# Optimization experiments

Hardware: AMD Instinct MI355X
Metric: run time of the kernel (lower is better)

## Reference

```python
import jax, jax.numpy as jnp
import numpy as np

B, T, D, H = 4096, 100, 64, 128
N_RK4 = 4  # fixed RK4 substeps per observation gap (deterministic stand-in for adaptive odeint)


def setup_inputs() -> dict:
    key = jax.random.key(0)
    ks = jax.random.split(key, 12)
    x_seq = jax.random.normal(ks[0], (B, T, D), dtype=jnp.float32)
    # strictly increasing shared timestamps (source only uses t_seq[0, :])
    t0 = jnp.cumsum(jax.random.uniform(ks[1], (T,), dtype=jnp.float32) * 0.1 + 0.01)
    t_seq = jnp.broadcast_to(t0, (B, T))
    s_h = 1.0 / np.sqrt(H)
    s_d = 1.0 / np.sqrt(D)
    # ODE func: f(h) = tanh(h W1^T + b1) W2^T + b2
    W1 = jax.random.normal(ks[2], (H, H), jnp.float32) * s_h
    b1 = jnp.zeros((H,), jnp.float32)
    W2 = jax.random.normal(ks[3], (H, H), jnp.float32) * s_h * 0.1
    b2 = jnp.zeros((H,), jnp.float32)
    # GRUCell params (PyTorch layout: [3H, in])
    W_ih = jax.random.normal(ks[4], (3 * H, D), jnp.float32) * s_d
    W_hh = jax.random.normal(ks[5], (3 * H, H), jnp.float32) * s_h
    b_ih = jax.random.normal(ks[6], (3 * H,), jnp.float32) * s_h
    b_hh = jax.random.normal(ks[7], (3 * H,), jnp.float32) * s_h
    W_mu = jax.random.normal(ks[8], (H, H), jnp.float32) * s_h
    b_mu = jnp.zeros((H,), jnp.float32)
    W_lv = jax.random.normal(ks[9], (H, H), jnp.float32) * s_h
    b_lv = jnp.zeros((H,), jnp.float32)
    return dict(x_seq=x_seq, t_seq=t_seq, W1=W1, b1=b1, W2=W2, b2=b2,
                W_ih=W_ih, W_hh=W_hh, b_ih=b_ih, b_hh=b_hh,
                W_mu=W_mu, b_mu=b_mu, W_lv=W_lv, b_lv=b_lv)


def _odernn(x_seq, t_seq, W1, b1, W2, b2, W_ih, W_hh, b_ih, b_hh, W_mu, b_mu, W_lv, b_lv):
    Hdim = W1.shape[0]

    def f(h):  # ode_func, autonomous
        return jnp.tanh(h @ W1.T + b1) @ W2.T + b2

    def rk4_jump(h, dt):  # integrate dh/dt = f(h) over dt with N_RK4 substeps
        sub = dt / N_RK4  # scalar
        for _ in range(N_RK4):
            k1 = f(h)
            k2 = f(h + 0.5 * sub * k1)
            k3 = f(h + 0.5 * sub * k2)
            k4 = f(h + sub * k3)
            h = h + (sub / 6.0) * (k1 + 2.0 * k2 + 2.0 * k3 + k4)
        return h

    def gru(x, h):
        gi = x @ W_ih.T + b_ih  # [B, 3H]
        gh = h @ W_hh.T + b_hh
        i_r, i_z, i_n = jnp.split(gi, 3, axis=-1)
        h_r, h_z, h_n = jnp.split(gh, 3, axis=-1)
        r = jax.nn.sigmoid(i_r + h_r)
        z = jax.nn.sigmoid(i_z + h_z)
        n = jnp.tanh(i_n + r * h_n)
        return (1.0 - z) * n + z * h

    t0 = t_seq[0]  # [T] shared times, as in source (t_seq[0, i])
    dt = jnp.concatenate([jnp.zeros((1,), t0.dtype), t0[1:] - t0[:-1]])  # dt[0]=0 -> no jump at i=0
    h0 = jnp.zeros((x_seq.shape[0], Hdim), x_seq.dtype)

    def step(h, inp):
        x_i, dt_i = inp
        h = rk4_jump(h, dt_i)
        h = gru(x_i, h)
        return h, None

    h, _ = jax.lax.scan(step, h0, (jnp.swapaxes(x_seq, 0, 1), dt))
    mu = h @ W_mu.T + b_mu
    logvar = h @ W_lv.T + b_lv
    return mu, logvar


def reference(x_seq, t_seq, W1, b1, W2, b2, W_ih, W_hh, b_ih, b_hh, W_mu, b_mu, W_lv, b_lv):
    return _odernn(x_seq, t_seq, W1, b1, W2, b2, W_ih, W_hh, b_ih, b_hh, W_mu, b_mu, W_lv, b_lv)
```

## Files before the change

### kernel.cpp

```cpp
#include <hip/hip_runtime.h>

#define Bn 4096
#define Tn 100
#define Dn 64
#define Hn 128

typedef _Float16 half8v __attribute__((ext_vector_type(8)));
typedef _Float16 half4v __attribute__((ext_vector_type(4)));
typedef float    float4v __attribute__((ext_vector_type(4)));
typedef float    float2v __attribute__((ext_vector_type(2)));

__device__ __forceinline__ float fast_tanh(float x) {
    float e = __expf(x + x);
    return 1.0f - 2.0f * __builtin_amdgcn_rcpf(e + 1.0f);
}
__device__ __forceinline__ float fast_sig(float x) {
    return __builtin_amdgcn_rcpf(1.0f + __expf(-x));
}
__device__ __forceinline__ float4v tanh4(float4v u) {
    float4v a;
#pragma unroll
    for (int r = 0; r < 4; r++) a[r] = fast_tanh(u[r]);
    return a;
}
__device__ __forceinline__ half4v pack4(float4v v) {
    half4v p;
#pragma unroll
    for (int r = 0; r < 4; r++) p[r] = (_Float16)v[r];
    return p;
}

__device__ __forceinline__ half8v load_wfrag(const float* __restrict__ W, int ld, int n, int k) {
    const float* p = W + (size_t)n * ld + k;
    float4v a = *(const float4v*)p;
    float4v b = *(const float4v*)(p + 4);
    half8v r;
    r[0] = (_Float16)a[0]; r[1] = (_Float16)a[1]; r[2] = (_Float16)a[2]; r[3] = (_Float16)a[3];
    r[4] = (_Float16)b[0]; r[5] = (_Float16)b[1]; r[6] = (_Float16)b[2]; r[7] = (_Float16)b[3];
    return r;
}

__global__ __launch_bounds__(512) void odernn_kernel(
    const float* __restrict__ x_seq, const float* __restrict__ t_seq,
    const float* __restrict__ W1,   const float* __restrict__ b1,
    const float* __restrict__ W2,   const float* __restrict__ b2,
    const float* __restrict__ W_ih, const float* __restrict__ W_hh,
    const float* __restrict__ b_ih, const float* __restrict__ b_hh,
    const float* __restrict__ W_mu, const float* __restrict__ b_mu,
    const float* __restrict__ W_lv, const float* __restrict__ b_lv,
    float* __restrict__ out)
{
    __shared__ _Float16 vbuf[16 * 136];
    __shared__ _Float16 abuf[2][16 * 136];
    __shared__ _Float16 xbuf[16 * 72];
    __shared__ float    ts_l[Tn];
    __shared__ float    c1s[Hn];

    const int tid  = threadIdx.x;
    const int lane = tid & 63;
    const int w    = tid >> 6;
    const int q    = lane >> 4;
    const int m    = lane & 15;
    const int blk  = blockIdx.x;

    if (tid < Tn) ts_l[tid] = t_seq[tid];
    for (int i = tid; i < 16 * 136; i += 512) vbuf[i] = (_Float16)0.f;
    if (tid < Hn) {
        float acc = 0.f;
        const float* r1 = W1 + (size_t)tid * Hn;
#pragma unroll 4
        for (int j = 0; j < Hn; j++) acc += b2[j] * r1[j];
        c1s[tid] = acc;
    }

    const int n0 = 16 * w + m;
    half8v w1f[4], w2f[4], whhf[3][4], wihf[3][2];
#pragma unroll
    for (int kt = 0; kt < 4; kt++) {
        w1f[kt] = load_wfrag(W1, Hn, n0, 32 * kt + q * 8);
        w2f[kt] = load_wfrag(W2, Hn, n0, 32 * kt + q * 8);
    }
#pragma unroll
    for (int g = 0; g < 3; g++) {
        int n = 128 * g + n0;
#pragma unroll
        for (int kt = 0; kt < 4; kt++) whhf[g][kt] = load_wfrag(W_hh, Hn, n, 32 * kt + q * 8);
#pragma unroll
        for (int kt = 0; kt < 2; kt++) wihf[g][kt] = load_wfrag(W_ih, Dn, n, 32 * kt + q * 8);
    }
    float4v b1q = *(const float4v*)(b1 + 16 * w + q * 4);
    float4v b2q = *(const float4v*)(b2 + 16 * w + q * 4);
    float4v bihq[3], bhhq[3];
#pragma unroll
    for (int g = 0; g < 3; g++) {
        bihq[g] = *(const float4v*)(b_ih + 128 * g + 16 * w + q * 4);
        bhhq[g] = *(const float4v*)(b_hh + 128 * g + 16 * w + q * 4);
    }

    float4v accM[4][2];
#pragma unroll
    for (int kt = 0; kt < 4; kt++) {
        float4v zz = {0.f, 0.f, 0.f, 0.f};
        accM[kt][0] = zz; accM[kt][1] = zz;
    }
    {
        const float* w1row = W1 + (size_t)n0 * Hn;
        for (int j = 0; j < Hn; j++) {
            float w1v = w1row[j];
            const float* w2r = W2 + (size_t)j * Hn + q * 8;
#pragma unroll
            for (int kt = 0; kt < 4; kt++) {
                float4v aa = *(const float4v*)(w2r + 32 * kt);
                float4v bb = *(const float4v*)(w2r + 32 * kt + 4);
#pragma unroll
                for (int r = 0; r < 4; r++) {
                    accM[kt][0][r] += w1v * aa[r];
                    accM[kt][1][r] += w1v * bb[r];
                }
            }
        }
    }
    half8v w21f[4];
#pragma unroll
    for (int kt = 0; kt < 4; kt++) {
#pragma unroll
        for (int r = 0; r < 4; r++) {
            w21f[kt][r]     = (_Float16)accM[kt][0][r];
            w21f[kt][r + 4] = (_Float16)accM[kt][1][r];
        }
    }

    float4v h = {0.f, 0.f, 0.f, 0.f};

    const int xrow = tid >> 5;
    const int xcol = (tid & 31) * 2;
    const float* xptr = x_seq + (size_t)(blk * 16 + xrow) * (Tn * Dn) + xcol;
    float2v xreg = *(const float2v*)xptr;

    const int wslot = m * 136 + 16 * w + q * 4;

    auto gemm4 = [&](const half8v* Wf, const _Float16* base, float4v cin) -> float4v {
        const _Float16* p = base + m * 136 + q * 8;
        half8v bf0 = *(const half8v*)(p);
        half8v bf1 = *(const half8v*)(p + 32);
        half8v bf2 = *(const half8v*)(p + 64);
        half8v bf3 = *(const half8v*)(p + 96);
        float4v o1 = cin;
        float4v o2 = {0.f, 0.f, 0.f, 0.f};
        o1 = __builtin_amdgcn_mfma_f32_16x16x32_f16(Wf[0], bf0, o1, 0, 0, 0);
        o2 = __builtin_amdgcn_mfma_f32_16x16x32_f16(Wf[2], bf2, o2, 0, 0, 0);
        o1 = __builtin_amdgcn_mfma_f32_16x16x32_f16(Wf[1], bf1, o1, 0, 0, 0);
        o2 = __builtin_amdgcn_mfma_f32_16x16x32_f16(Wf[3], bf3, o2, 0, 0, 0);
#pragma unroll
        for (int r = 0; r < 4; r++) o1[r] += o2[r];
        return o1;
    };

    float4v c1q;
    __syncthreads();
#pragma unroll
    for (int r = 0; r < 4; r++) c1q[r] = c1s[16 * w + q * 4 + r];
    const float4v zero4 = {0.f, 0.f, 0.f, 0.f};

#pragma unroll 1
    for (int t = 0; t < Tn; ++t) {
        {
            _Float16* xp = xbuf + xrow * 72 + xcol;
            xp[0] = (_Float16)xreg[0]; xp[1] = (_Float16)xreg[1];
        }
        float tc  = ts_l[t];
        float tp  = (t > 0) ? ts_l[t - 1] : tc;
        float sub = (tc - tp) * 0.25f;
        float hs  = 0.5f * sub;
        float s6  = sub * (1.0f / 6.0f);
        __syncthreads();
        if (t + 1 < Tn) xreg = *(const float2v*)(xptr + (t + 1) * Dn);

        float4v gi[3];
        {
            const _Float16* xp = xbuf + m * 72 + q * 8;
            half8v xf0 = *(const half8v*)(xp);
            half8v xf1 = *(const half8v*)(xp + 32);
#pragma unroll
            for (int g = 0; g < 3; g++) {
                float4v acc = bihq[g];
                acc = __builtin_amdgcn_mfma_f32_16x16x32_f16(wihf[g][0], xf0, acc, 0, 0, 0);
                acc = __builtin_amdgcn_mfma_f32_16x16x32_f16(wihf[g][1], xf1, acc, 0, 0, 0);
                gi[g] = acc;
            }
        }
        float4v u_h = gemm4(w1f, vbuf, b1q);

        if (sub != 0.0f) {
            float4v Abar = zero4;
#pragma unroll 1
            for (int s = 0; s < 4; s++) {
                float4v a1 = tanh4(u_h);
                float4v A  = a1;
                *(half4v*)(abuf[0] + wslot) = pack4(a1);
                __syncthreads();
                float4v g = gemm4(w21f, abuf[0], c1q);
                float4v u;
#pragma unroll
                for (int r = 0; r < 4; r++) u[r] = u_h[r] + hs * g[r];
                float4v a2 = tanh4(u);
#pragma unroll
                for (int r = 0; r < 4; r++) A[r] += 2.0f * a2[r];
                *(half4v*)(abuf[1] + wslot) = pack4(a2);
                __syncthreads();
                g = gemm4(w21f, abuf[1], c1q);
#pragma unroll
                for (int r = 0; r < 4; r++) u[r] = u_h[r] + hs * g[r];
                float4v a3 = tanh4(u);
#pragma unroll
                for (int r = 0; r < 4; r++) A[r] += 2.0f * a3[r];
                *(half4v*)(abuf[0] + wslot) = pack4(a3);
                __syncthreads();
                g = gemm4(w21f, abuf[0], c1q);
#pragma unroll
                for (int r = 0; r < 4; r++) u[r] = u_h[r] + sub * g[r];
                float4v a4 = tanh4(u);
#pragma unroll
                for (int r = 0; r < 4; r++) A[r] += a4[r];
                *(half4v*)(abuf[1] + wslot) = pack4(A);
                __syncthreads();
                g = gemm4(w21f, abuf[1], zero4);
#pragma unroll
                for (int r = 0; r < 4; r++) {
                    u_h[r]  += s6 * g[r] + sub * c1q[r];
                    Abar[r] += A[r];
                }
            }
            *(half4v*)(abuf[0] + wslot) = pack4(Abar);
            __syncthreads();
            float4v gw = gemm4(w2f, abuf[0], zero4);
            float fourSub = 4.0f * sub;
#pragma unroll
            for (int r = 0; r < 4; r++) h[r] += s6 * gw[r] + fourSub * b2q[r];
            *(half4v*)(vbuf + wslot) = pack4(h);
            __syncthreads();
        }

        float4v gh[3];
        {
            const _Float16* p = vbuf + m * 136 + q * 8;
            half8v bf0 = *(const half8v*)(p);
            half8v bf1 = *(const half8v*)(p + 32);
            half8v bf2 = *(const half8v*)(p + 64);
            half8v bf3 = *(const half8v*)(p + 96);
#pragma unroll
            for (int g = 0; g < 3; g++) {
                float4v acc = bhhq[g];
                acc = __builtin_amdgcn_mfma_f32_16x16x32_f16(whhf[g][0], bf0, acc, 0, 0, 0);
                acc = __builtin_amdgcn_mfma_f32_16x16x32_f16(whhf[g][1], bf1, acc, 0, 0, 0);
                acc = __builtin_amdgcn_mfma_f32_16x16x32_f16(whhf[g][2], bf2, acc, 0, 0, 0);
                acc = __builtin_amdgcn_mfma_f32_16x16x32_f16(whhf[g][3], bf3, acc, 0, 0, 0);
                gh[g] = acc;
            }
        }
        __syncthreads();

        {
            half4v pk;
#pragma unroll
            for (int r = 0; r < 4; r++) {
                float rr = fast_sig(gi[0][r] + gh[0][r]);
                float zz = fast_sig(gi[1][r] + gh[1][r]);
                float nn = fast_tanh(gi[2][r] + rr * gh[2][r]);
                float hv = (1.0f - zz) * nn + zz * h[r];
                h[r] = hv;
                pk[r] = (_Float16)hv;
            }
            *(half4v*)(vbuf + wslot) = pk;
        }
    }

    __syncthreads();

#pragma unroll
    for (int mat = 0; mat < 2; mat++) {
        const float* Wm = mat ? W_lv : W_mu;
        const float* bm = mat ? b_lv : b_mu;
        float4v acc = *(const float4v*)(bm + 16 * w + q * 4);
        const _Float16* p = vbuf + m * 136 + q * 8;
#pragma unroll
        for (int kt = 0; kt < 4; kt++) {
            half8v af = load_wfrag(Wm, Hn, n0, 32 * kt + q * 8);
            acc = __builtin_amdgcn_mfma_f32_16x16x32_f16(af, *(const half8v*)(p + kt * 32), acc, 0, 0, 0);
        }
        *(float4v*)(out + (size_t)mat * Bn * Hn + (size_t)(blk * 16 + m) * Hn + 16 * w + q * 4) = acc;
    }
}

extern "C" void kernel_launch(void* const* d_in, const int* in_sizes, int n_in,
                              void* d_out, int out_size, void* d_ws, size_t ws_size,
                              hipStream_t stream) {
    (void)in_sizes; (void)n_in; (void)d_ws; (void)ws_size; (void)out_size;
    odernn_kernel<<<dim3(Bn / 16), dim3(512), 0, stream>>>(
        (const float*)d_in[0],  (const float*)d_in[1],  (const float*)d_in[2],
        (const float*)d_in[3],  (const float*)d_in[4],  (const float*)d_in[5],
        (const float*)d_in[6],  (const float*)d_in[7],  (const float*)d_in[8],
        (const float*)d_in[9],  (const float*)d_in[10], (const float*)d_in[11],
        (const float*)d_in[12], (const float*)d_in[13], (float*)d_out);
}
```

Before: 815.6 us.

## Halve batch rows per block to 8, raise occupancy, use raw LDS barriers

Each block now handles 8 batch rows instead of 16 and launches twice as many blocks. The MFMA B-operand rows are duplicated (m&7), so half of each 16-wide MFMA column does redundant work. The aim is to spread the latency-bound serial recurrence across more blocks and CUs. Launch bounds now request 4 blocks per SM, and __syncthreads is replaced by an inline s_waitcnt lgkmcnt(0)+s_barrier to cut barrier overhead. The cost is twice the total MFMA work and the weight-fragment setup per block, plus register pressure from the occupancy hint.

Measured after the change: 2.063 ms. 153% more time.

```diff
diff --git a/kernel.cpp b/kernel.cpp
--- a/kernel.cpp
+++ b/kernel.cpp
@@ -4,11 +4,13 @@
 #define Tn 100
 #define Dn 64
 #define Hn 128
+#define ROWS 8
 
 typedef _Float16 half8v __attribute__((ext_vector_type(8)));
 typedef _Float16 half4v __attribute__((ext_vector_type(4)));
 typedef float    float4v __attribute__((ext_vector_type(4)));
-typedef float    float2v __attribute__((ext_vector_type(2)));
+
+#define BAR() asm volatile("s_waitcnt lgkmcnt(0)\ns_barrier" ::: "memory")
 
 __device__ __forceinline__ float fast_tanh(float x) {
     float e = __expf(x + x);
@@ -40,7 +42,7 @@
     return r;
 }
 
-__global__ __launch_bounds__(512) void odernn_kernel(
+__global__ __launch_bounds__(512, 4) void odernn_kernel(
     const float* __restrict__ x_seq, const float* __restrict__ t_seq,
     const float* __restrict__ W1,   const float* __restrict__ b1,
     const float* __restrict__ W2,   const float* __restrict__ b2,
@@ -52,7 +54,7 @@
 {
     __shared__ _Float16 vbuf[16 * 136];
     __shared__ _Float16 abuf[2][16 * 136];
-    __shared__ _Float16 xbuf[16 * 72];
+    __shared__ _Float16 xbuf[ROWS * 72];
     __shared__ float    ts_l[Tn];
     __shared__ float    c1s[Hn];
 
@@ -61,6 +63,7 @@
     const int w    = tid >> 6;
     const int q    = lane >> 4;
     const int m    = lane & 15;
+    const int rowm = m & 7;
     const int blk  = blockIdx.x;
 
     if (tid < Tn) ts_l[tid] = t_seq[tid];
@@ -132,15 +135,16 @@
 
     float4v h = {0.f, 0.f, 0.f, 0.f};
 
-    const int xrow = tid >> 5;
-    const int xcol = (tid & 31) * 2;
-    const float* xptr = x_seq + (size_t)(blk * 16 + xrow) * (Tn * Dn) + xcol;
-    float2v xreg = *(const float2v*)xptr;
+    const int xrow = tid >> 6;
+    const int xcol = tid & 63;
+    const float* xptr = x_seq + (size_t)(blk * ROWS + xrow) * (Tn * Dn) + xcol;
+    float xreg = *xptr;
 
     const int wslot = m * 136 + 16 * w + q * 4;
+    const int rslot = rowm * 136 + q * 8;
 
     auto gemm4 = [&](const half8v* Wf, const _Float16* base, float4v cin) -> float4v {
-        const _Float16* p = base + m * 136 + q * 8;
+        const _Float16* p = base + rslot;
         half8v bf0 = *(const half8v*)(p);
         half8v bf1 = *(const half8v*)(p + 32);
         half8v bf2 = *(const half8v*)(p + 64);
@@ -157,28 +161,25 @@
     };
 
     float4v c1q;
-    __syncthreads();
+    BAR();
 #pragma unroll
     for (int r = 0; r < 4; r++) c1q[r] = c1s[16 * w + q * 4 + r];
     const float4v zero4 = {0.f, 0.f, 0.f, 0.f};
 
 #pragma unroll 1
     for (int t = 0; t < Tn; ++t) {
-        {
-            _Float16* xp = xbuf + xrow * 72 + xcol;
-            xp[0] = (_Float16)xreg[0]; xp[1] = (_Float16)xreg[1];
-        }
+        xbuf[xrow * 72 + xcol] = (_Float16)xreg;
         float tc  = ts_l[t];
         float tp  = (t > 0) ? ts_l[t - 1] : tc;
         float sub = (tc - tp) * 0.25f;
         float hs  = 0.5f * sub;
         float s6  = sub * (1.0f / 6.0f);
-        __syncthreads();
-        if (t + 1 < Tn) xreg = *(const float2v*)(xptr + (t + 1) * Dn);
+        BAR();
+        if (t + 1 < Tn) xreg = xptr[(t + 1) * Dn];
 
         float4v gi[3];
         {
-            const _Float16* xp = xbuf + m * 72 + q * 8;
+            const _Float16* xp = xbuf + rowm * 72 + q * 8;
             half8v xf0 = *(const half8v*)(xp);
             half8v xf1 = *(const half8v*)(xp + 32);
 #pragma unroll
@@ -198,7 +199,7 @@
                 float4v a1 = tanh4(u_h);
                 float4v A  = a1;
                 *(half4v*)(abuf[0] + wslot) = pack4(a1);
-                __syncthreads();
+                BAR();
                 float4v g = gemm4(w21f, abuf[0], c1q);
                 float4v u;
 #pragma unroll
@@ -207,7 +208,7 @@
 #pragma unroll
                 for (int r = 0; r < 4; r++) A[r] += 2.0f * a2[r];
                 *(half4v*)(abuf[1] + wslot) = pack4(a2);
-                __syncthreads();
+                BAR();
                 g = gemm4(w21f, abuf[1], c1q);
 #pragma unroll
                 for (int r = 0; r < 4; r++) u[r] = u_h[r] + hs * g[r];
@@ -215,7 +216,7 @@
 #pragma unroll
                 for (int r = 0; r < 4; r++) A[r] += 2.0f * a3[r];
                 *(half4v*)(abuf[0] + wslot) = pack4(a3);
-                __syncthreads();
+                BAR();
                 g = gemm4(w21f, abuf[0], c1q);
 #pragma unroll
                 for (int r = 0; r < 4; r++) u[r] = u_h[r] + sub * g[r];
@@ -223,7 +224,7 @@
 #pragma unroll
                 for (int r = 0; r < 4; r++) A[r] += a4[r];
                 *(half4v*)(abuf[1] + wslot) = pack4(A);
-                __syncthreads();
+                BAR();
                 g = gemm4(w21f, abuf[1], zero4);
 #pragma unroll
                 for (int r = 0; r < 4; r++) {
@@ -232,18 +233,18 @@
                 }
             }
             *(half4v*)(abuf[0] + wslot) = pack4(Abar);
-            __syncthreads();
+            BAR();
             float4v gw = gemm4(w2f, abuf[0], zero4);
             float fourSub = 4.0f * sub;
 #pragma unroll
             for (int r = 0; r < 4; r++) h[r] += s6 * gw[r] + fourSub * b2q[r];
             *(half4v*)(vbuf + wslot) = pack4(h);
-            __syncthreads();
+            BAR();
         }
 
         float4v gh[3];
         {
-            const _Float16* p = vbuf + m * 136 + q * 8;
+            const _Float16* p = vbuf + rslot;
             half8v bf0 = *(const half8v*)(p);
             half8v bf1 = *(const half8v*)(p + 32);
             half8v bf2 = *(const half8v*)(p + 64);
@@ -258,7 +259,7 @@
                 gh[g] = acc;
             }
         }
-        __syncthreads();
+        BAR();
 
         {
             half4v pk;
@@ -275,20 +276,22 @@
         }
     }
 
-    __syncthreads();
+    BAR();
 
 #pragma unroll
     for (int mat = 0; mat < 2; mat++) {
         const float* Wm = mat ? W_lv : W_mu;
         const float* bm = mat ? b_lv : b_mu;
         float4v acc = *(const float4v*)(bm + 16 * w + q * 4);
-        const _Float16* p = vbuf + m * 136 + q * 8;
+        const _Float16* p = vbuf + rslot;
 #pragma unroll
         for (int kt = 0; kt < 4; kt++) {
             half8v af = load_wfrag(Wm, Hn, n0, 32 * kt + q * 8);
             acc = __builtin_amdgcn_mfma_f32_16x16x32_f16(af, *(const half8v*)(p + kt * 32), acc, 0, 0, 0);
         }
-        *(float4v*)(out + (size_t)mat * Bn * Hn + (size_t)(blk * 16 + m) * Hn + 16 * w + q * 4) = acc;
+        if (m < ROWS) {
+            *(float4v*)(out + (size_t)mat * Bn * Hn + (size_t)(blk * ROWS + m) * Hn + 16 * w + q * 4) = acc;
+        }
     }
 }
 
@@ -296,7 +299,7 @@
                               void* d_out, int out_size, void* d_ws, size_t ws_size,
                               hipStream_t stream) {
     (void)in_sizes; (void)n_in; (void)d_ws; (void)ws_size; (void)out_size;
-    odernn_kernel<<<dim3(Bn / 16), dim3(512), 0, stream>>>(
+    odernn_kernel<<<dim3(Bn / ROWS), dim3(512), 0, stream>>>(
         (const float*)d_in[0],  (const float*)d_in[1],  (const float*)d_in[2],
         (const float*)d_in[3],  (const float*)d_in[4],  (const float*)d_in[5],
         (const float*)d_in[6],  (const float*)d_in[7],  (const float*)d_in[8],
```
